# Kernel tuning notes

Hardware: AMD Instinct MI355X
Metric: run time of the kernel (lower is better)

Reference implementation:

```python
import jax, jax.numpy as jnp
import numpy as np

D_MODEL = 1024
D_STATE = 128
HEAD_DIM = 64
EXPAND = 2
K = 4  # conv_kernel
N_GROUPS = 1
D_INNER = EXPAND * D_MODEL            # 2048
N_HEADS = D_INNER // HEAD_DIM         # 32
D_PROJ = 2 * D_INNER + 2 * N_GROUPS * D_STATE + N_HEADS  # 4384
EPS = 1e-6


def _rmsnorm(x, w):
    return x * jax.lax.rsqrt(jnp.mean(x * x, axis=-1, keepdims=True) + EPS) * w


def setup_inputs() -> dict:
    key = jax.random.key(0)
    ks = jax.random.split(key, 8)
    B, L = 2, 2048
    x = jax.random.normal(ks[0], (B, L, D_MODEL), jnp.float32)
    norm_w = jnp.ones((D_MODEL,), jnp.float32)
    in_proj_w = jax.random.normal(ks[1], (D_PROJ, D_MODEL), jnp.float32) / np.sqrt(D_MODEL).astype(np.float32)
    conv_w = jax.random.normal(ks[2], (D_INNER, K), jnp.float32) / np.sqrt(K).astype(np.float32)
    conv_b = jnp.zeros((D_INNER,), jnp.float32)
    A_log = jnp.log(jax.random.uniform(ks[3], (N_HEADS,), jnp.float32) * 15.0 + 1.0)
    D = jnp.ones((N_HEADS,), jnp.float32)
    dt_bias = jnp.log(jax.random.uniform(ks[4], (N_HEADS,), jnp.float32) * 0.099 + 0.001)
    out_proj_w = jax.random.normal(ks[5], (D_MODEL, D_INNER), jnp.float32) / np.sqrt(D_INNER).astype(np.float32)
    return dict(x=x, norm_w=norm_w, in_proj_w=in_proj_w, conv_w=conv_w, conv_b=conv_b,
                A_log=A_log, D=D, dt_bias=dt_bias, out_proj_w=out_proj_w)


def reference(x, norm_w, in_proj_w, conv_w, conv_b, A_log, D, dt_bias, out_proj_w):
    batch, L, _ = x.shape
    residual = x
    xn = _rmsnorm(x, norm_w)
    proj = jnp.einsum('bld,pd->blp', xn, in_proj_w)  # (B,L,D_PROJ)

    # split fused projection -> z, x_ssm, B, C, dt_raw
    i = 0
    z = proj[:, :, i:i + D_INNER]; i += D_INNER
    x_ssm = proj[:, :, i:i + D_INNER]; i += D_INNER
    bc = N_GROUPS * D_STATE
    Bm = proj[:, :, i:i + bc].reshape(batch, L, N_GROUPS, D_STATE); i += bc
    Cm = proj[:, :, i:i + bc].reshape(batch, L, N_GROUPS, D_STATE); i += bc
    dt_raw = proj[:, :, i:i + N_HEADS]

    # causal depthwise conv1d (left-pad K-1) + SiLU
    xp = jnp.pad(x_ssm, ((0, 0), (K - 1, 0), (0, 0)))
    x_conv = conv_b
    for k in range(K):
        x_conv = x_conv + xp[:, k:k + L, :] * conv_w[:, k]
    x_conv = jax.nn.silu(x_conv)

    xh = x_conv.reshape(batch, L, N_HEADS, HEAD_DIM)
    dt = jax.nn.softplus(dt_raw + dt_bias)          # (B,L,H)
    dA = jnp.exp(-jnp.exp(A_log) * dt)              # (B,L,H)
    dtx = dt[..., None] * xh                        # (B,L,H,P)

    gidx = jnp.arange(N_HEADS) // (N_HEADS // N_GROUPS)
    Bg = Bm[:, :, gidx, :]                          # (B,L,H,N)
    Cg = Cm[:, :, gidx, :]                          # (B,L,H,N)

    def step(h, inp):
        dA_t, dtx_t, B_t, C_t = inp                 # (B,H), (B,H,P), (B,H,N), (B,H,N)
        h = h * dA_t[:, :, None, None] + dtx_t[..., None] * B_t[:, :, None, :]
        y_t = jnp.einsum('bhpn,bhn->bhp', h, C_t)
        return h, y_t

    h0 = jnp.zeros((batch, N_HEADS, HEAD_DIM, D_STATE), jnp.float32)
    xs = (jnp.swapaxes(dA, 0, 1), jnp.swapaxes(dtx, 0, 1),
          jnp.swapaxes(Bg, 0, 1), jnp.swapaxes(Cg, 0, 1))
    _, ys = jax.lax.scan(step, h0, xs)              # ys: (L,B,H,P)
    y = jnp.swapaxes(ys, 0, 1) + D[None, None, :, None] * xh

    y = y.reshape(batch, L, D_INNER) * jax.nn.silu(z)
    return residual + jnp.einsum('bli,di->bld', y, out_proj_w)
```

## Files before the change

### kernel.cpp

```cpp
#include <hip/hip_runtime.h>
#include <hip/hip_bf16.h>

#define L_SEQ 2048
#define DM 1024
#define DI 2048
#define DS 128
#define NH 32
#define HD 64
#define DPROJ 4384
#define DPAD 4480
#define NBATCH 2
#define NCH 8
#define CH 256
#define B_OFF 4096
#define C_OFF 4224
#define DT_OFF 4352
#define SWZ(row) ((((row) ^ ((row) >> 3)) & 7) << 4)

typedef unsigned short u16;
typedef __attribute__((ext_vector_type(8))) short short8;
typedef __attribute__((ext_vector_type(4))) float f32x4;

#define GLL16(g, l)                                                     \
  __builtin_amdgcn_global_load_lds(                                     \
      (const __attribute__((address_space(1))) unsigned int*)(g),       \
      (__attribute__((address_space(3))) unsigned int*)(l), 16, 0, 0)
#define SBAR __builtin_amdgcn_s_barrier()
#define MEMFENCE asm volatile("" ::: "memory")

__device__ __forceinline__ u16 f2bf(float f) {
  union { float f; unsigned u; } c; c.f = f;
  unsigned u = c.u;
  u += 0x7fffu + ((u >> 16) & 1u);
  return (u16)(u >> 16);
}
__device__ __forceinline__ float bf2f(u16 u) {
  return __uint_as_float((unsigned)u << 16);
}
__device__ __forceinline__ float siluf(float x) {
  return x / (1.0f + expf(-x));
}
__device__ __forceinline__ void store_out(u16* C, size_t o, float v) { C[o] = f2bf(v); }
__device__ __forceinline__ void store_out(float* C, size_t o, float v) { C[o] = v; }

__global__ __launch_bounds__(256) void prep_kernel(
    const float* __restrict__ x, const float* __restrict__ norm_w,
    const float* __restrict__ w1, const float* __restrict__ w2,
    u16* __restrict__ xnb, u16* __restrict__ w1b, u16* __restrict__ w2b,
    int M) {
  int bidx = blockIdx.x;
  int t = threadIdx.x;
  if (bidx < M) {
    const float* row = x + (size_t)bidx * DM;
    float4 v = *(const float4*)(row + t * 4);
    float ss = v.x * v.x + v.y * v.y + v.z * v.z + v.w * v.w;
#pragma unroll
    for (int o = 32; o > 0; o >>= 1) ss += __shfl_xor(ss, o);
    __shared__ float sred[4];
    if ((t & 63) == 0) sred[t >> 6] = ss;
    __syncthreads();
    ss = sred[0] + sred[1] + sred[2] + sred[3];
    float rs = rsqrtf(ss * (1.0f / DM) + 1e-6f);
    float4 wv = *(const float4*)(norm_w + t * 4);
    ushort4 o;
    o.x = f2bf(v.x * rs * wv.x);
    o.y = f2bf(v.y * rs * wv.y);
    o.z = f2bf(v.z * rs * wv.z);
    o.w = f2bf(v.w * rs * wv.w);
    *(ushort4*)(xnb + (size_t)bidx * DM + t * 4) = o;
  } else if (bidx < M + DPAD) {
    int r = bidx - M;
    int c = t * 4;
    ushort4 u;
    if (r < DPROJ) {
      float4 v = *(const float4*)(w1 + (size_t)r * DM + c);
      u.x = f2bf(v.x); u.y = f2bf(v.y); u.z = f2bf(v.z); u.w = f2bf(v.w);
    } else {
      u.x = 0; u.y = 0; u.z = 0; u.w = 0;
    }
    *(ushort4*)(w1b + (size_t)r * DM + c) = u;
  } else {
    size_t i = ((size_t)(bidx - M - DPAD) * 256 + t) * 8;
    float4 v0 = *(const float4*)(w2 + i);
    float4 v1 = *(const float4*)(w2 + i + 4);
    ushort4 a, b;
    a.x = f2bf(v0.x); a.y = f2bf(v0.y); a.z = f2bf(v0.z); a.w = f2bf(v0.w);
    b.x = f2bf(v1.x); b.y = f2bf(v1.y); b.z = f2bf(v1.z); b.w = f2bf(v1.w);
    *(ushort4*)(w2b + i) = a;
    *(ushort4*)(w2b + i + 4) = b;
  }
}

template <typename OT, bool RES, bool DTS, int BN, int SPLIT>
__global__ __launch_bounds__(256, 4) void gemm_bt(
    const u16* __restrict__ A, const u16* __restrict__ Bw,
    OT* __restrict__ C, const float* __restrict__ resid,
    float* __restrict__ dts, int M, int N, int Kloop, int LDA, int nbx) {
  constexpr int WN = BN / 2;
  constexpr int NJ = WN / 16;
  __shared__ u16 lA[2][128 * 32];
  __shared__ u16 lB[2][BN * 32];
  const int tid = threadIdx.x;
  const int wv = tid >> 6, lane = tid & 63;
  const int wm = wv >> 1, wn = wv & 1;

  const int nwg = gridDim.x;
  const int cpx = nwg >> 3;
  const int wg = blockIdx.x;
  const int swz = (wg & 7) * cpx + (wg >> 3);
  int kh = 0, tile = swz;
  if (SPLIT == 2) { kh = swz & 1; tile = swz >> 1; }
  const int m0 = (tile / nbx) * 128, n0 = (tile % nbx) * BN;

  const u16* Ab = A + (size_t)kh * Kloop;
  const u16* Bb = Bw + (size_t)kh * Kloop;
  OT* Cb = (SPLIT == 2) ? (C + (size_t)kh * M * N) : C;

  const int rowS = tid >> 2;
  const int colS = (tid & 3) * 8;
  const u16* gA0 = Ab + (size_t)(m0 + rowS) * LDA + colS;
  const u16* gA1 = Ab + (size_t)(m0 + rowS + 64) * LDA + colS;
  const u16* gB0 = Bb + (size_t)(n0 + rowS) * LDA + colS;
  const u16* gB1 = Bb + (size_t)(n0 + rowS + 64) * LDA + colS;

  auto stage = [&](int kt, int buf) {
    const int ko = kt << 5;
    GLL16(gA0 + ko, &lA[buf][wv * 512]);
    GLL16(gA1 + ko, &lA[buf][2048 + wv * 512]);
    GLL16(gB0 + ko, &lB[buf][wv * 512]);
    if (BN == 128) GLL16(gB1 + ko, &lB[buf][2048 + wv * 512]);
  };

  f32x4 acc[4][NJ] = {};
  const int r = lane & 15;
  const int koff = (lane >> 4) * 8;

  auto compute = [&](int buf) {
    short8 af[4], bfr[NJ];
#pragma unroll
    for (int i = 0; i < 4; ++i)
      af[i] = *(const short8*)&lA[buf][(wm * 64 + i * 16 + r) * 32 + koff];
#pragma unroll
    for (int j = 0; j < NJ; ++j)
      bfr[j] = *(const short8*)&lB[buf][(wn * WN + j * 16 + r) * 32 + koff];
#pragma unroll
    for (int i = 0; i < 4; ++i)
#pragma unroll
      for (int j = 0; j < NJ; ++j)
        acc[i][j] = __builtin_amdgcn_mfma_f32_16x16x32_bf16(
            af[i], bfr[j], acc[i][j], 0, 0, 0);
  };

  const int nk = Kloop >> 5;
  stage(0, 0);
  for (int kt = 0; kt < nk; ++kt) {
    const int b = kt & 1;
    asm volatile("s_waitcnt vmcnt(0)" ::: "memory");
    SBAR;
    MEMFENCE;
    if (kt + 1 < nk) stage(kt + 1, b ^ 1);
    compute(b);
  }

  const int rbase = m0 + wm * 64 + (lane >> 4) * 4;
  const int cbase = n0 + wn * WN + (lane & 15);
#pragma unroll
  for (int i = 0; i < 4; ++i) {
#pragma unroll
    for (int j = 0; j < NJ; ++j) {
      int row0 = rbase + i * 16;
      int col = cbase + j * 16;
#pragma unroll
      for (int rr = 0; rr < 4; ++rr) {
        size_t o = (size_t)(row0 + rr) * N + col;
        float v = acc[i][j][rr];
        if (RES) v += resid[o];
        store_out(Cb, o, v);
        if (DTS) {
          if (col >= DT_OFF && col < DT_OFF + NH)
            dts[(size_t)(row0 + rr) * NH + (col - DT_OFF)] = v;
        }
      }
    }
  }
}

__global__ __launch_bounds__(256) void add_out_kernel(
    const float* __restrict__ x, const float* __restrict__ p,
    float* __restrict__ out) {
  size_t i = ((size_t)blockIdx.x * 256 + threadIdx.x) * 8;
  const float* p1 = p + (size_t)4096 * 1024;
#pragma unroll
  for (int q = 0; q < 2; ++q) {
    float4 a = *(const float4*)(x + i + q * 4);
    float4 b = *(const float4*)(p + i + q * 4);
    float4 c = *(const float4*)(p1 + i + q * 4);
    float4 o;
    o.x = a.x + b.x + c.x; o.y = a.y + b.y + c.y;
    o.z = a.z + b.z + c.z; o.w = a.w + b.w + c.w;
    *(float4*)(out + i + q * 4) = o;
  }
}

__global__ __launch_bounds__(512) void scan_state_mfma(
    const u16* __restrict__ proj, const float* __restrict__ dts,
    const float* __restrict__ dt_bias, const float* __restrict__ A_log,
    const float* __restrict__ cw, const float* __restrict__ cb,
    u16* __restrict__ xhy, float* __restrict__ dAdt,
    float* __restrict__ S, float* __restrict__ P) {
  __shared__ u16 sBT[128 * 64];
  __shared__ u16 sXT[64 * 64];
  __shared__ u16 sXW[64 * 64];
  __shared__ float sDt[64], sCum[64], sWs[64], sLam[64];

  const int bid = blockIdx.x;
  const int ch = bid & 7, hh = (bid >> 3) & 31, b = bid >> 8;
  const int tid = threadIdx.x;
  const int w = tid >> 6, l = tid & 63;
  const int tw = w >> 1, half = w & 1;
  const int klane = (l >> 4) * 16;
  const size_t mchunk = (size_t)(b * L_SEQ + ch * CH);

  const int cvp0 = (tid & 7) * 8;
  float4 cwv[8];
  float cbv[8];
#pragma unroll
  for (int j = 0; j < 8; ++j) {
    cwv[j] = *(const float4*)(cw + (size_t)(hh * 64 + cvp0 + j) * 4);
    cbv[j] = cb[hh * 64 + cvp0 + j];
  }
  const float dtb_h = dt_bias[hh];
  const float eAh = expf(A_log[hh]);

  f32x4 hAcc[4] = {};
  float ctot = 0.0f;

  auto STAGE = [&](int sc) {
    const size_t m0 = mchunk + (size_t)sc * 64;
    {
      const int tp = tid >> 4;
      const int n0 = (tid & 15) * 8;
      const u16* r0 = proj + (m0 + 2 * tp) * DPAD + B_OFF + n0;
      short8 lo8 = *(const short8*)r0;
      short8 hi8 = *(const short8*)(r0 + DPAD);
#pragma unroll
      for (int q = 0; q < 8; ++q) {
        int n = n0 + q;
        unsigned v = (unsigned)(u16)lo8[q] | ((unsigned)(u16)hi8[q] << 16);
        *(unsigned*)((char*)sBT + ((n * 128 + 4 * tp) ^ SWZ(n))) = v;
      }
    }
    {
      const int sx = tid >> 3;
      const int gm = (int)m0 + sx;
      const int lrow = gm & (L_SEQ - 1);
      float accv[8];
#pragma unroll
      for (int j = 0; j < 8; ++j) accv[j] = cbv[j];
#pragma unroll
      for (int k = 0; k < 4; ++k) {
        if (lrow + k >= 3) {
          short8 rv = *(const short8*)(proj + (size_t)(gm + k - 3) * DPAD + DI +
                                       hh * 64 + cvp0);
#pragma unroll
          for (int j = 0; j < 8; ++j) {
            float wk = (k == 0) ? cwv[j].x : (k == 1) ? cwv[j].y
                      : (k == 2) ? cwv[j].z : cwv[j].w;
            accv[j] = fmaf(bf2f((u16)rv[j]), wk, accv[j]);
          }
        }
      }
      short8 o;
#pragma unroll
      for (int i = 0; i < 8; ++i) {
        u16 bv = f2bf(siluf(accv[i]));
        o[i] = (short)bv;
        int p = cvp0 + i;
        *(u16*)((char*)sXT + ((p * 128 + 2 * sx) ^ SWZ(p))) = bv;
      }
      *(short8*)(xhy + (size_t)gm * DI + hh * 64 + cvp0) = o;
    }
    if (tid < 64) {
      float raw = dts[(m0 + tid) * NH + hh] + dtb_h;
      float dtv = fmaxf(raw, 0.0f) + log1pf(expf(-fabsf(raw)));
      float a = -eAh * dtv;
      float2 ad; ad.x = a; ad.y = dtv;
      *(float2*)(dAdt + (m0 + tid) * 64 + hh * 2) = ad;
      sDt[tid] = dtv;
      float val = a;
#pragma unroll
      for (int o = 1; o < 64; o <<= 1) {
        float t2 = __shfl_up(val, o);
        if (tid >= o) val += t2;
      }
      sCum[tid] = val;
      float c63 = __shfl(val, 63);
      sWs[tid] = __expf(c63 - val) * dtv;
      sLam[tid] = __expf(val);
    }
  };

  STAGE(0);
  __syncthreads();

  for (int sc = 0; sc < 4; ++sc) {
    {
      int p = tid >> 3, sg = tid & 7;
      int byteX = (p * 128 + sg * 16) ^ SWZ(p);
      short8 xv = *(short8*)((char*)sXT + byteX);
      short8 outp;
#pragma unroll
      for (int j = 0; j < 8; ++j)
        outp[j] = (short)f2bf(bf2f((u16)xv[j]) * sWs[sg * 8 + j]);
      *(short8*)((char*)sXW + byteX) = outp;
    }
    __syncthreads();

    {
      float lam63 = sLam[63];
      ctot += sCum[63];
#pragma unroll
      for (int j = 0; j < 4; ++j) {
        hAcc[j][0] *= lam63; hAcc[j][1] *= lam63;
        hAcc[j][2] *= lam63; hAcc[j][3] *= lam63;
      }
      int prow = tw * 16 + (l & 15);
      short8 aXW[2];
#pragma unroll
      for (int kk = 0; kk < 2; ++kk)
        aXW[kk] = *(short8*)((char*)sXW + ((prow * 128 + kk * 64 + klane) ^ SWZ(prow)));
#pragma unroll
      for (int j = 0; j < 4; ++j) {
        int nrow = (half * 4 + j) * 16 + (l & 15);
#pragma unroll
        for (int kk = 0; kk < 2; ++kk) {
          short8 bBT = *(short8*)((char*)sBT + ((nrow * 128 + kk * 64 + klane) ^ SWZ(nrow)));
          hAcc[j] = __builtin_amdgcn_mfma_f32_16x16x32_bf16(aXW[kk], bBT, hAcc[j], 0, 0, 0);
        }
      }
    }
    __syncthreads();
    if (sc < 3) STAGE(sc + 1);
    __syncthreads();
  }

  float* Sb = S + (size_t)((b * 32 + hh) * NCH + ch) * 8192;
  const int p0 = tw * 16 + (l >> 4) * 4;
#pragma unroll
  for (int j = 0; j < 4; ++j) {
    int n = (half * 4 + j) * 16 + (l & 15);
#pragma unroll
    for (int r = 0; r < 4; ++r)
      Sb[(p0 + r) * 128 + n] = hAcc[j][r];
  }
  if (tid == 0) P[(b * 32 + hh) * NCH + ch] = __expf(ctot);
}

__global__ __launch_bounds__(256) void combine_kernel(
    float* __restrict__ S, const float* __restrict__ P) {
  int tid = blockIdx.x * 256 + threadIdx.x;
  int bh = tid >> 13, pn = tid & 8191;
  size_t base = (size_t)bh * NCH * 8192 + pn;
  float E = 0.0f;
#pragma unroll
  for (int c = 0; c < NCH; ++c) {
    size_t o = base + (size_t)c * 8192;
    float Sc = S[o];
    S[o] = E;
    E = fmaf(P[bh * NCH + c], E, Sc);
  }
}

__global__ __launch_bounds__(512) void scan_y_mfma(
    const u16* __restrict__ proj, const float* __restrict__ dAdt,
    const u16* __restrict__ xhy, const float* __restrict__ Dv,
    const float* __restrict__ S, u16* __restrict__ yb) {
  __shared__ u16 sC[64 * 128];
  __shared__ u16 sB[64 * 128];
  __shared__ u16 sHb[64 * 128];
  __shared__ u16 sBT[128 * 64];
  __shared__ u16 sXT[64 * 64];
  __shared__ u16 sXW[64 * 64];
  __shared__ u16 sW[64 * 64];
  __shared__ float sDt[64], sCum[64], sWs[64], sLam[64];

  const int bid = blockIdx.x;
  const int ch = bid & 7, hh = (bid >> 3) & 31, b = bid >> 8;
  const int tid = threadIdx.x;
  const int w = tid >> 6, l = tid & 63;
  const int tw = w >> 1, half = w & 1;
  const int klane = (l >> 4) * 16;
  const float Dh = Dv[hh];
  const size_t mchunk = (size_t)(b * L_SEQ + ch * CH);

  f32x4 hAcc[4];
  {
    const float* Sb = S + (size_t)((b * 32 + hh) * NCH + ch) * 8192;
    const int p0 = tw * 16 + (l >> 4) * 4;
#pragma unroll
    for (int j = 0; j < 4; ++j) {
      int n = (half * 4 + j) * 16 + (l & 15);
#pragma unroll
      for (int r = 0; r < 4; ++r)
        hAcc[j][r] = Sb[(p0 + r) * 128 + n];
    }
    int p = tid >> 3, sg = tid & 7;
#pragma unroll
    for (int i = 0; i < 4; ++i) {
      float4 v = *(const float4*)(Sb + p * 128 + sg * 16 + 4 * i);
      ushort4 u;
      u.x = f2bf(v.x); u.y = f2bf(v.y); u.z = f2bf(v.z); u.w = f2bf(v.w);
      *(ushort4*)((char*)sHb + ((p * 256 + (sg * 16 + 4 * i) * 2) ^ SWZ(p))) = u;
    }
  }

  auto STAGE = [&](int sc) {
    const size_t m0 = mchunk + (size_t)sc * 64;
    {
      const int tp = tid >> 4;
      const int n0 = (tid & 15) * 8;
      const u16* r0 = proj + (m0 + 2 * tp) * DPAD;
      short8 b0 = *(const short8*)(r0 + B_OFF + n0);
      short8 b1 = *(const short8*)(r0 + DPAD + B_OFF + n0);
      short8 c0v = *(const short8*)(r0 + C_OFF + n0);
      short8 c1v = *(const short8*)(r0 + DPAD + C_OFF + n0);
      *(short8*)((char*)sB + ((2 * tp * 256 + n0 * 2) ^ SWZ(2 * tp))) = b0;
      *(short8*)((char*)sB + (((2 * tp + 1) * 256 + n0 * 2) ^ SWZ(2 * tp + 1))) = b1;
      *(short8*)((char*)sC + ((2 * tp * 256 + n0 * 2) ^ SWZ(2 * tp))) = c0v;
      *(short8*)((char*)sC + (((2 * tp + 1) * 256 + n0 * 2) ^ SWZ(2 * tp + 1))) = c1v;
#pragma unroll
      for (int q = 0; q < 8; ++q) {
        int n = n0 + q;
        unsigned v = (unsigned)(u16)b0[q] | ((unsigned)(u16)b1[q] << 16);
        *(unsigned*)((char*)sBT + ((n * 128 + 4 * tp) ^ SWZ(n))) = v;
      }
    }
    {
      const int sx = tid >> 3;
      const int p0 = (tid & 7) * 8;
      short8 xv8 = *(const short8*)(xhy + (m0 + sx) * DI + hh * 64 + p0);
#pragma unroll
      for (int i = 0; i < 8; ++i) {
        int p = p0 + i;
        *(u16*)((char*)sXT + ((p * 128 + 2 * sx) ^ SWZ(p))) = (u16)xv8[i];
      }
    }
    if (tid < 64) {
      float2 ad = *(const float2*)(dAdt + (m0 + tid) * 64 + hh * 2);
      float a = ad.x, dtv = ad.y;
      sDt[tid] = dtv;
      float val = a;
#pragma unroll
      for (int o = 1; o < 64; o <<= 1) {
        float t2 = __shfl_up(val, o);
        if (tid >= o) val += t2;
      }
      sCum[tid] = val;
      float c63 = __shfl(val, 63);
      sWs[tid] = __expf(c63 - val) * dtv;
      sLam[tid] = __expf(val);
    }
  };

  STAGE(0);
  __syncthreads();

  for (int sc = 0; sc < 4; ++sc) {
    const size_t m0 = mchunk + (size_t)sc * 64;
    {
      int p = tid >> 3, sg = tid & 7;
      int byteX = (p * 128 + sg * 16) ^ SWZ(p);
      short8 xv = *(short8*)((char*)sXT + byteX);
      short8 outp;
#pragma unroll
      for (int j = 0; j < 8; ++j)
        outp[j] = (short)f2bf(bf2f((u16)xv[j]) * sWs[sg * 8 + j]);
      *(short8*)((char*)sXW + byteX) = outp;
    }
    __syncthreads();

    const int trow = tw * 16 + (l & 15);
    short8 aC[4];
#pragma unroll
    for (int kk = 0; kk < 4; ++kk)
      aC[kk] = *(short8*)((char*)sC + ((trow * 256 + kk * 64 + klane) ^ SWZ(trow)));

    {
      f32x4 g[2] = {};
#pragma unroll
      for (int sv2 = 0; sv2 < 2; ++sv2) {
        int srow = (half * 2 + sv2) * 16 + (l & 15);
#pragma unroll
        for (int kk = 0; kk < 4; ++kk) {
          short8 bB = *(short8*)((char*)sB + ((srow * 256 + kk * 64 + klane) ^ SWZ(srow)));
          g[sv2] = __builtin_amdgcn_mfma_f32_16x16x32_bf16(aC[kk], bB, g[sv2], 0, 0, 0);
        }
      }
#pragma unroll
      for (int sv2 = 0; sv2 < 2; ++sv2) {
        int s = (half * 2 + sv2) * 16 + (l & 15);
        float dts_ = sDt[s], cums = sCum[s];
#pragma unroll
        for (int r = 0; r < 4; ++r) {
          int t = tw * 16 + (l >> 4) * 4 + r;
          float v = (t >= s) ? g[sv2][r] * __expf(sCum[t] - cums) * dts_ : 0.0f;
          *(u16*)((char*)sW + ((t * 128 + 2 * s) ^ SWZ(t))) = f2bf(v);
        }
      }
    }
    __syncthreads();

    f32x4 y1[2] = {}, y2[2] = {};
    float lamv[4], lam63 = sLam[63];
#pragma unroll
    for (int r = 0; r < 4; ++r) lamv[r] = sLam[tw * 16 + (l >> 4) * 4 + r];
    {
      short8 aW[2];
#pragma unroll
      for (int kk = 0; kk < 2; ++kk)
        aW[kk] = *(short8*)((char*)sW + ((trow * 128 + kk * 64 + klane) ^ SWZ(trow)));
#pragma unroll
      for (int pv2 = 0; pv2 < 2; ++pv2) {
        int prow = (half * 2 + pv2) * 16 + (l & 15);
#pragma unroll
        for (int kk = 0; kk < 2; ++kk) {
          short8 bX = *(short8*)((char*)sXT + ((prow * 128 + kk * 64 + klane) ^ SWZ(prow)));
          y1[pv2] = __builtin_amdgcn_mfma_f32_16x16x32_bf16(aW[kk], bX, y1[pv2], 0, 0, 0);
        }
#pragma unroll
        for (int kk = 0; kk < 4; ++kk) {
          short8 bH = *(short8*)((char*)sHb + ((prow * 256 + kk * 64 + klane) ^ SWZ(prow)));
          y2[pv2] = __builtin_amdgcn_mfma_f32_16x16x32_bf16(aC[kk], bH, y2[pv2], 0, 0, 0);
        }
      }
#pragma unroll
      for (int j = 0; j < 4; ++j) {
        hAcc[j][0] *= lam63; hAcc[j][1] *= lam63;
        hAcc[j][2] *= lam63; hAcc[j][3] *= lam63;
      }
      short8 aXW[2];
#pragma unroll
      for (int kk = 0; kk < 2; ++kk)
        aXW[kk] = *(short8*)((char*)sXW + ((trow * 128 + kk * 64 + klane) ^ SWZ(trow)));
#pragma unroll
      for (int j = 0; j < 4; ++j) {
        int nrow = (half * 4 + j) * 16 + (l & 15);
#pragma unroll
        for (int kk = 0; kk < 2; ++kk) {
          short8 bBT = *(short8*)((char*)sBT + ((nrow * 128 + kk * 64 + klane) ^ SWZ(nrow)));
          hAcc[j] = __builtin_amdgcn_mfma_f32_16x16x32_bf16(aXW[kk], bBT, hAcc[j], 0, 0, 0);
        }
      }
    }
    __syncthreads();

    {
#pragma unroll
      for (int j = 0; j < 4; ++j) {
        int n = (half * 4 + j) * 16 + (l & 15);
#pragma unroll
        for (int r = 0; r < 4; ++r) {
          int p = tw * 16 + (l >> 4) * 4 + r;
          *(u16*)((char*)sHb + ((p * 256 + 2 * n) ^ SWZ(p))) = f2bf(hAcc[j][r]);
        }
      }
#pragma unroll
      for (int pv2 = 0; pv2 < 2; ++pv2) {
        int p = (half * 2 + pv2) * 16 + (l & 15);
#pragma unroll
        for (int r = 0; r < 4; ++r) {
          int t = tw * 16 + (l >> 4) * 4 + r;
          int col = hh * 64 + p;
          size_t gy = (m0 + t) * DI + col;
          float xv = bf2f(xhy[gy]);
          float yv = y1[pv2][r] + lamv[r] * y2[pv2][r] + Dh * xv;
          float zv = bf2f(proj[(m0 + t) * DPAD + col]);
          yb[gy] = f2bf(yv * siluf(zv));
        }
      }
      if (sc < 3) STAGE(sc + 1);
    }
    __syncthreads();
  }
}

extern "C" void kernel_launch(void* const* d_in, const int* in_sizes, int n_in,
                              void* d_out, int out_size, void* d_ws, size_t ws_size,
                              hipStream_t stream) {
  const float* x      = (const float*)d_in[0];
  const float* norm_w = (const float*)d_in[1];
  const float* w1     = (const float*)d_in[2];
  const float* cw     = (const float*)d_in[3];
  const float* cb     = (const float*)d_in[4];
  const float* A_log  = (const float*)d_in[5];
  const float* Dv     = (const float*)d_in[6];
  const float* dt_b   = (const float*)d_in[7];
  const float* w2     = (const float*)d_in[8];
  float* out = (float*)d_out;

  char* ws = (char*)d_ws;
  u16*   xnb  = (u16*)(ws);
  u16*   w1b  = (u16*)(ws + 8388608);
  u16*   w2b  = (u16*)(ws + 17563648);
  u16*   proj = (u16*)(ws + 21757952);
  float* dts  = (float*)(ws + 58458112);
  u16*   xhy  = (u16*)(ws + 58982400);
  float* dAdt = (float*)(ws + 75759616);
  u16*   yb   = (u16*)(ws + 76808192);
  float* S    = (float*)(ws + 93585408);
  float* part = (float*)(ws + 93585408);
  float* P    = (float*)(ws + 127139840);

  const int M = NBATCH * L_SEQ;

  prep_kernel<<<M + DPAD + 1024, 256, 0, stream>>>(
      x, norm_w, w1, w2, xnb, w1b, w2b, M);
  gemm_bt<u16, false, true, 128, 1><<<(DPAD / 128) * (M / 128), 256, 0, stream>>>(
      xnb, w1b, proj, nullptr, dts, M, DPAD, DM, DM, DPAD / 128);
  scan_state_mfma<<<512, 512, 0, stream>>>(
      proj, dts, dt_b, A_log, cw, cb, xhy, dAdt, S, P);
  combine_kernel<<<2048, 256, 0, stream>>>(S, P);
  scan_y_mfma<<<512, 512, 0, stream>>>(proj, dAdt, xhy, Dv, S, yb);
  gemm_bt<float, false, false, 64, 2><<<2 * (DM / 64) * (M / 128), 256, 0, stream>>>(
      yb, w2b, part, nullptr, nullptr, M, DM, DI / 2, DI, DM / 64);
  add_out_kernel<<<M * DM / 2048, 256, 0, stream>>>(x, part, out);
}
```

Before: 192.9 us.

## Recompute conv+SiLU in scan_y and fold residual into split-K GEMM

The scan_state kernel no longer writes the conv+SiLU output (xhy) to global memory. scan_y recomputes the causal conv from proj and reuses the smem copy for the D-skip term, which removes an 8 MB write and its later reads at the cost of repeating the conv arithmetic. The residual add moves into the first split-K half of the output GEMM epilogue, so add_out_kernel reads one fewer input stream. The workspace layout is compacted to match.

```diff
diff --git a/kernel.cpp b/kernel.cpp
--- a/kernel.cpp
+++ b/kernel.cpp
@@ -115,6 +115,7 @@
   const u16* Ab = A + (size_t)kh * Kloop;
   const u16* Bb = Bw + (size_t)kh * Kloop;
   OT* Cb = (SPLIT == 2) ? (C + (size_t)kh * M * N) : C;
+  const float* rb = (RES && kh == 0) ? resid : nullptr;
 
   const int rowS = tid >> 2;
   const int colS = (tid & 3) * 8;
@@ -174,7 +175,7 @@
       for (int rr = 0; rr < 4; ++rr) {
         size_t o = (size_t)(row0 + rr) * N + col;
         float v = acc[i][j][rr];
-        if (RES) v += resid[o];
+        if (RES) { if (rb) v += rb[o]; }
         store_out(Cb, o, v);
         if (DTS) {
           if (col >= DT_OFF && col < DT_OFF + NH)
@@ -186,18 +187,16 @@
 }
 
 __global__ __launch_bounds__(256) void add_out_kernel(
-    const float* __restrict__ x, const float* __restrict__ p,
-    float* __restrict__ out) {
+    const float* __restrict__ p, float* __restrict__ out) {
   size_t i = ((size_t)blockIdx.x * 256 + threadIdx.x) * 8;
   const float* p1 = p + (size_t)4096 * 1024;
 #pragma unroll
   for (int q = 0; q < 2; ++q) {
-    float4 a = *(const float4*)(x + i + q * 4);
     float4 b = *(const float4*)(p + i + q * 4);
     float4 c = *(const float4*)(p1 + i + q * 4);
     float4 o;
-    o.x = a.x + b.x + c.x; o.y = a.y + b.y + c.y;
-    o.z = a.z + b.z + c.z; o.w = a.w + b.w + c.w;
+    o.x = b.x + c.x; o.y = b.y + c.y;
+    o.z = b.z + c.z; o.w = b.w + c.w;
     *(float4*)(out + i + q * 4) = o;
   }
 }
@@ -206,8 +205,7 @@
     const u16* __restrict__ proj, const float* __restrict__ dts,
     const float* __restrict__ dt_bias, const float* __restrict__ A_log,
     const float* __restrict__ cw, const float* __restrict__ cb,
-    u16* __restrict__ xhy, float* __restrict__ dAdt,
-    float* __restrict__ S, float* __restrict__ P) {
+    float* __restrict__ dAdt, float* __restrict__ S, float* __restrict__ P) {
   __shared__ u16 sBT[128 * 64];
   __shared__ u16 sXT[64 * 64];
   __shared__ u16 sXW[64 * 64];
@@ -270,15 +268,12 @@
           }
         }
       }
-      short8 o;
 #pragma unroll
       for (int i = 0; i < 8; ++i) {
         u16 bv = f2bf(siluf(accv[i]));
-        o[i] = (short)bv;
         int p = cvp0 + i;
         *(u16*)((char*)sXT + ((p * 128 + 2 * sx) ^ SWZ(p))) = bv;
       }
-      *(short8*)(xhy + (size_t)gm * DI + hh * 64 + cvp0) = o;
     }
     if (tid < 64) {
       float raw = dts[(m0 + tid) * NH + hh] + dtb_h;
@@ -373,8 +368,9 @@
 
 __global__ __launch_bounds__(512) void scan_y_mfma(
     const u16* __restrict__ proj, const float* __restrict__ dAdt,
-    const u16* __restrict__ xhy, const float* __restrict__ Dv,
-    const float* __restrict__ S, u16* __restrict__ yb) {
+    const float* __restrict__ cw, const float* __restrict__ cb,
+    const float* __restrict__ Dv, const float* __restrict__ S,
+    u16* __restrict__ yb) {
   __shared__ u16 sC[64 * 128];
   __shared__ u16 sB[64 * 128];
   __shared__ u16 sHb[64 * 128];
@@ -392,6 +388,15 @@
   const int klane = (l >> 4) * 16;
   const float Dh = Dv[hh];
   const size_t mchunk = (size_t)(b * L_SEQ + ch * CH);
+
+  const int cvp0 = (tid & 7) * 8;
+  float4 cwv[8];
+  float cbv[8];
+#pragma unroll
+  for (int j = 0; j < 8; ++j) {
+    cwv[j] = *(const float4*)(cw + (size_t)(hh * 64 + cvp0 + j) * 4);
+    cbv[j] = cb[hh * 64 + cvp0 + j];
+  }
 
   f32x4 hAcc[4];
   {
@@ -437,12 +442,29 @@
     }
     {
       const int sx = tid >> 3;
-      const int p0 = (tid & 7) * 8;
-      short8 xv8 = *(const short8*)(xhy + (m0 + sx) * DI + hh * 64 + p0);
+      const int gm = (int)m0 + sx;
+      const int lrow = gm & (L_SEQ - 1);
+      float accv[8];
+#pragma unroll
+      for (int j = 0; j < 8; ++j) accv[j] = cbv[j];
+#pragma unroll
+      for (int k = 0; k < 4; ++k) {
+        if (lrow + k >= 3) {
+          short8 rv = *(const short8*)(proj + (size_t)(gm + k - 3) * DPAD + DI +
+                                       hh * 64 + cvp0);
+#pragma unroll
+          for (int j = 0; j < 8; ++j) {
+            float wk = (k == 0) ? cwv[j].x : (k == 1) ? cwv[j].y
+                      : (k == 2) ? cwv[j].z : cwv[j].w;
+            accv[j] = fmaf(bf2f((u16)rv[j]), wk, accv[j]);
+          }
+        }
+      }
 #pragma unroll
       for (int i = 0; i < 8; ++i) {
-        int p = p0 + i;
-        *(u16*)((char*)sXT + ((p * 128 + 2 * sx) ^ SWZ(p))) = (u16)xv8[i];
+        u16 bv = f2bf(siluf(accv[i]));
+        int p = cvp0 + i;
+        *(u16*)((char*)sXT + ((p * 128 + 2 * sx) ^ SWZ(p))) = bv;
       }
     }
     if (tid < 64) {
@@ -485,6 +507,17 @@
     for (int kk = 0; kk < 4; ++kk)
       aC[kk] = *(short8*)((char*)sC + ((trow * 256 + kk * 64 + klane) ^ SWZ(trow)));
 
+    float xreg[2][4];
+#pragma unroll
+    for (int pv2 = 0; pv2 < 2; ++pv2) {
+      int p = (half * 2 + pv2) * 16 + (l & 15);
+#pragma unroll
+      for (int r = 0; r < 4; ++r) {
+        int t = tw * 16 + (l >> 4) * 4 + r;
+        xreg[pv2][r] = bf2f(*(const u16*)((char*)sXT + ((p * 128 + 2 * t) ^ SWZ(p))));
+      }
+    }
+
     {
       f32x4 g[2] = {};
 #pragma unroll
@@ -572,8 +605,7 @@
           int t = tw * 16 + (l >> 4) * 4 + r;
           int col = hh * 64 + p;
           size_t gy = (m0 + t) * DI + col;
-          float xv = bf2f(xhy[gy]);
-          float yv = y1[pv2][r] + lamv[r] * y2[pv2][r] + Dh * xv;
+          float yv = y1[pv2][r] + lamv[r] * y2[pv2][r] + Dh * xreg[pv2][r];
           float zv = bf2f(proj[(m0 + t) * DPAD + col]);
           yb[gy] = f2bf(yv * siluf(zv));
         }
@@ -604,12 +636,11 @@
   u16*   w2b  = (u16*)(ws + 17563648);
   u16*   proj = (u16*)(ws + 21757952);
   float* dts  = (float*)(ws + 58458112);
-  u16*   xhy  = (u16*)(ws + 58982400);
+  u16*   yb   = (u16*)(ws + 58982400);
   float* dAdt = (float*)(ws + 75759616);
-  u16*   yb   = (u16*)(ws + 76808192);
-  float* S    = (float*)(ws + 93585408);
-  float* part = (float*)(ws + 93585408);
-  float* P    = (float*)(ws + 127139840);
+  float* S    = (float*)(ws + 76808192);
+  float* part = (float*)(ws + 76808192);
+  float* P    = (float*)(ws + 110362624);
 
   const int M = NBATCH * L_SEQ;
 
@@ -618,10 +649,10 @@
   gemm_bt<u16, false, true, 128, 1><<<(DPAD / 128) * (M / 128), 256, 0, stream>>>(
       xnb, w1b, proj, nullptr, dts, M, DPAD, DM, DM, DPAD / 128);
   scan_state_mfma<<<512, 512, 0, stream>>>(
-      proj, dts, dt_b, A_log, cw, cb, xhy, dAdt, S, P);
+      proj, dts, dt_b, A_log, cw, cb, dAdt, S, P);
   combine_kernel<<<2048, 256, 0, stream>>>(S, P);
-  scan_y_mfma<<<512, 512, 0, stream>>>(proj, dAdt, xhy, Dv, S, yb);
-  gemm_bt<float, false, false, 64, 2><<<2 * (DM / 64) * (M / 128), 256, 0, stream>>>(
-      yb, w2b, part, nullptr, nullptr, M, DM, DI / 2, DI, DM / 64);
-  add_out_kernel<<<M * DM / 2048, 256, 0, stream>>>(x, part, out);
-}
+  scan_y_mfma<<<512, 512, 0, stream>>>(proj, dAdt, cw, cb, Dv, S, yb);
+  gemm_bt<float, true, false, 64, 2><<<2 * (DM / 64) * (M / 128), 256, 0, stream>>>(
+      yb, w2b, part, x, nullptr, M, DM, DI / 2, DI, DM / 64);
+  add_out_kernel<<<M * DM / 2048, 256, 0, stream>>>(part, out);
+}
```

Result: slower. 210.5 us (+9.1%).
